# Optimization experiments

Measured on AMD Instinct MI355X. Metric: run time of the kernel, lower is better.

## Reference

```python
import jax, jax.numpy as jnp
import numpy as np
from functools import partial

GRID = 5  # 224/32 - 2
N_ANCHORS = 3
N_BOX = GRID * GRID * N_ANCHORS  # 75


def _make_anchors():
    # faithful replication of _create_anchors (grid-index cx,cy with pixel-scale w,h)
    scales = [56, 112, 224]
    a = np.zeros((GRID, GRID, N_ANCHORS, 8), np.float32)
    for x in range(GRID):
        for y in range(GRID):
            for k in range(N_ANCHORS):
                w = h = scales[k]
                a[x, y, k] = [x - w // 2, y - h // 2, x + w // 2, y + h // 2, x, y, w, h]
    return jnp.asarray(a)

ANCHORS = _make_anchors()  # [5,5,3,8]: x0,y0,x1,y1,cx,cy,w,h


def conv2d(x, w, b, pad):
    y = jax.lax.conv_general_dilated(x, w, (1, 1), [(pad, pad), (pad, pad)],
                                     dimension_numbers=('NCHW', 'OIHW', 'NCHW'))
    return y + b[None, :, None, None]


def maxpool2(x):
    return jax.lax.reduce_window(x, -jnp.inf, jax.lax.max,
                                 (1, 1, 2, 2), (1, 1, 2, 2), 'VALID')


def deparam_bboxes(rp_reg):
    # rp_reg: [B,5,5,3,4]; anchors broadcast over batch
    aw = ANCHORS[..., 6]; ah = ANCHORS[..., 7]
    ax = ANCHORS[..., 4]; ay = ANCHORS[..., 5]
    cx = rp_reg[..., 0] * aw + ax
    cy = rp_reg[..., 1] * ah + ay
    w = jnp.exp(rp_reg[..., 2]) * aw
    h = jnp.exp(rp_reg[..., 3]) * ah
    return jnp.stack([cx - w / 2, cy - h / 2, cx + w / 2, cy + h / 2], axis=-1)


def _iou_as_written(bi, bj):
    # replicates bb_intersection_over_union EXACTLY, including the missing
    # parentheses bug: inter/areaA + areaB - inter
    xA = jnp.maximum(bi[0], bj[..., 0]); yA = jnp.maximum(bi[1], bj[..., 1])
    xB = jnp.minimum(bi[2], bj[..., 2]); yB = jnp.minimum(bi[3], bj[..., 3])
    inter = jnp.maximum(0.0, xB - xA + 1) * jnp.maximum(0.0, yB - yA + 1)
    areaA = (bi[2] - bi[0] + 1) * (bi[3] - bi[1] + 1)
    areaB = (bj[..., 2] - bj[..., 0] + 1) * (bj[..., 3] - bj[..., 1] + 1)
    return inter / areaA + areaB - inter


def nms_single(boxes, scores, thresh=0.7):
    # boxes [75,4], scores [75]; greedy suppression in score order (vectorized
    # replacement of the O(n^2) Python-loop NMS in _compute_bboxes)
    order = jnp.argsort(-scores)
    b = boxes[order]
    idx = jnp.arange(N_BOX)

    def body(i, keep):
        iou = _iou_as_written(b[i], b)          # [75]
        sup = (idx > i) & (iou > thresh) & keep[i]
        return keep & ~sup

    keep_sorted = jax.lax.fori_loop(0, N_BOX, body, jnp.ones(N_BOX, bool))
    return jnp.zeros(N_BOX, bool).at[order].set(keep_sorted)


def setup_inputs() -> dict:
    key = jax.random.key(0)
    ks = jax.random.split(key, 16)
    B = 32
    inp = {"x": jax.random.normal(ks[0], (B, 3, 224, 224), jnp.float32)}
    chans = [3, 64, 128, 256, 512, 512]
    for i in range(5):
        cin, cout = chans[i], chans[i + 1]
        std = float(np.sqrt(2.0 / (cout * 9)))  # kaiming fan_out, relu
        inp[f"fw{i}"] = jax.random.normal(ks[1 + i], (cout, cin, 3, 3), jnp.float32) * std
        inp[f"fb{i}"] = jnp.zeros((cout,), jnp.float32)
    # RPN heads: normal(0, 0.01), zero bias (per _initialize_rp_weights)
    inp["rpw_w"] = jax.random.normal(ks[6], (512, 512, 3, 3), jnp.float32) * 0.01
    inp["rpw_b"] = jnp.zeros((512,), jnp.float32)
    inp["cls_w"] = jax.random.normal(ks[7], (N_ANCHORS, 512, 1, 1), jnp.float32) * 0.01
    inp["cls_b"] = jnp.zeros((N_ANCHORS,), jnp.float32)
    inp["reg_w"] = jax.random.normal(ks[8], (4 * N_ANCHORS, 512, 1, 1), jnp.float32) * 0.01
    inp["reg_b"] = jnp.zeros((4 * N_ANCHORS,), jnp.float32)
    # classifier2: Linear(512*7*7, 20), normal(0, 0.01)
    inp["fc_w"] = jax.random.normal(ks[9], (20, 512 * 7 * 7), jnp.float32) * 0.01
    inp["fc_b"] = jnp.zeros((20,), jnp.float32)
    return inp


def reference(x, fw0, fb0, fw1, fb1, fw2, fb2, fw3, fb3, fw4, fb4,
              rpw_w, rpw_b, cls_w, cls_b, reg_w, reg_b, fc_w, fc_b):
    B = x.shape[0]
    feat = x
    for w, b in ((fw0, fb0), (fw1, fb1), (fw2, fb2), (fw3, fb3), (fw4, fb4)):
        feat = maxpool2(jax.nn.relu(conv2d(feat, w, b, pad=1)))
    # feat: [B,512,7,7]
    rp512 = jax.nn.relu(conv2d(feat, rpw_w, rpw_b, pad=0))          # [B,512,5,5]
    rp_cls = jax.nn.sigmoid(conv2d(rp512, cls_w, cls_b, pad=0))     # [B,3,5,5]
    rp_reg = conv2d(rp512, reg_w, reg_b, pad=0)                     # [B,12,5,5]
    # faithful to torch .view (row-major reshape, NOT permute)
    rp_cls = rp_cls.reshape(B, GRID, GRID, N_ANCHORS)
    rp_reg = rp_reg.reshape(B, GRID, GRID, N_ANCHORS, 4)
    bboxes = deparam_bboxes(rp_reg)                                 # [B,5,5,3,4]
    keep = jax.vmap(nms_single)(bboxes.reshape(B, N_BOX, 4),
                                rp_cls.reshape(B, N_BOX))           # [B,75] bool
    logits = feat.reshape(B, -1) @ fc_w.T + fc_b                    # [B,20]
    return logits, rp_cls, rp_reg, bboxes, keep
```

## Files before the change

### kernel.cpp

```cpp
#include <hip/hip_runtime.h>
#include <math.h>


#define OFF_LOGITS 0
#define OFF_CLS    640
#define OFF_REG    3040
#define OFF_BOXES  12640
#define OFF_KEEP   22240

constexpr int BATCH = 32;

typedef _Float16 h8 __attribute__((ext_vector_type(8)));
typedef _Float16 h4 __attribute__((ext_vector_type(4)));
typedef float    f4 __attribute__((ext_vector_type(4)));

#define MFMA16(a, b, c) __builtin_amdgcn_mfma_f32_16x16x32_f16(a, b, c, 0, 0, 0)

#if defined(__has_builtin)
#  if __has_builtin(__builtin_amdgcn_global_load_lds)
#    define HAS_GLL 1
#  endif
#endif

__device__ __forceinline__ void stage16(const _Float16* g, _Float16* lbase, int lane) {
#ifdef HAS_GLL
  __builtin_amdgcn_global_load_lds((const __attribute__((address_space(1))) void*)g,
                                   (__attribute__((address_space(3))) void*)lbase,
                                   16, 0, 0);
#else
  *reinterpret_cast<h8*>(lbase + lane * 8) = *reinterpret_cast<const h8*>(g);
#endif
}

constexpr size_t A_OFF = 0;
constexpr size_t B_OFF = 106463232;
constexpr size_t W_OFF = 161579008;
constexpr size_t P_OFF = A_OFF + 8388608;

constexpr int I0_E = 26615808;
constexpr int I1_E = 13778944;
constexpr int I2_E = 7372800;
constexpr int I3_E = 4194304;
constexpr int I4_E = 802816;

__global__ __launch_bounds__(256)
void wcvt(const float* __restrict__ src, _Float16* __restrict__ dHi,
          _Float16* __restrict__ dLo, int COUT, int CIN) {
  const int total = COUT * CIN * 9;
  for (int idx = blockIdx.x * 256 + threadIdx.x; idx < total; idx += gridDim.x * 256) {
    const int co = idx / (CIN * 9);
    const int r = idx % (CIN * 9);
    const int ci = r / 9, tap = r % 9;
    const float v = src[idx];
    const _Float16 h = (_Float16)v;
    const int o = ((tap * (CIN >> 5) + (ci >> 5)) * COUT + co) * 32 + (ci & 31);
    dHi[o] = h;
    dLo[o] = (_Float16)(v - (float)h);
  }
}

__global__ __launch_bounds__(256)
void zero_ring(_Float16* __restrict__ hi, _Float16* __restrict__ lo, int P, int C) {
  const int c8n = C / 8, cells = 4 * P - 4;
  const int tot = 32 * cells * c8n;
  for (int idx = blockIdx.x * 256 + threadIdx.x; idx < tot; idx += gridDim.x * 256) {
    const int c8 = idx % c8n;
    const int cell = (idx / c8n) % cells;
    const int n = idx / (c8n * cells);
    int y, xx;
    if (cell < 2 * P) { y = (cell < P) ? 0 : (P - 1); xx = cell % P; }
    else { const int q = cell - 2 * P; y = 1 + (q >> 1); xx = (q & 1) ? (P - 1) : 0; }
    const long o = ((long)(n * P + y) * P + xx) * C + c8 * 8;
    h8 z = {};
    *reinterpret_cast<h8*>(hi + o) = z;
    *reinterpret_cast<h8*>(lo + o) = z;
  }
}

__global__ __launch_bounds__(256)
void conv_l0(const float* __restrict__ x, const float* __restrict__ w0,
             const float* __restrict__ b0, _Float16* __restrict__ outHi,
             _Float16* __restrict__ outLo) {
  const int bid = blockIdx.x;
  const int tx0 = (bid % 7) * 16, ty0 = ((bid / 7) % 7) * 16, n = bid / 49;
  __shared__ float sIn[3 * 34 * 34];
  __shared__ float sW[1728];
  __shared__ float sB[64];
  const int tid = threadIdx.x;
  for (int idx = tid; idx < 3 * 34 * 34; idx += 256) {
    const int ci = idx / 1156, rem = idx % 1156, r = rem / 34, cc = rem % 34;
    const int y = 2 * ty0 - 1 + r, xx = 2 * tx0 - 1 + cc;
    float v = 0.f;
    if ((unsigned)y < 224u && (unsigned)xx < 224u)
      v = x[((n * 3 + ci) * 224 + y) * 224 + xx];
    sIn[idx] = v;
  }
  for (int idx = tid; idx < 1728; idx += 256) sW[idx] = w0[idx];
  if (tid < 64) sB[tid] = b0[tid];
  __syncthreads();

  const int tpy = tid / 16, tpx = tid % 16;
  float win[3][4][4];
  #pragma unroll
  for (int ci = 0; ci < 3; ++ci)
    #pragma unroll
    for (int dr = 0; dr < 4; ++dr)
      #pragma unroll
      for (int dc = 0; dc < 4; ++dc)
        win[ci][dr][dc] = sIn[ci * 1156 + (2 * tpy + dr) * 34 + (2 * tpx + dc)];

  const long ob = ((long)(n * 114 + ty0 + tpy + 1) * 114 + tx0 + tpx + 1) * 64;
  for (int co4 = 0; co4 < 16; ++co4) {
    h4 hh, ll;
    #pragma unroll
    for (int j = 0; j < 4; ++j) {
      const int co = co4 * 4 + j;
      float a00 = 0.f, a01 = 0.f, a10 = 0.f, a11 = 0.f;
      #pragma unroll
      for (int ci = 0; ci < 3; ++ci)
        #pragma unroll
        for (int ky = 0; ky < 3; ++ky)
          #pragma unroll
          for (int kx = 0; kx < 3; ++kx) {
            const float wv = sW[co * 27 + ci * 9 + ky * 3 + kx];
            a00 = fmaf(win[ci][ky][kx], wv, a00);
            a01 = fmaf(win[ci][ky][kx + 1], wv, a01);
            a10 = fmaf(win[ci][ky + 1][kx], wv, a10);
            a11 = fmaf(win[ci][ky + 1][kx + 1], wv, a11);
          }
      const float p = fmaxf(fmaxf(fmaxf(a00, a01), fmaxf(a10, a11)) + sB[co], 0.f);
      const _Float16 h = (_Float16)p;
      hh[j] = h;
      ll[j] = (_Float16)(p - (float)h);
    }
    *reinterpret_cast<h4*>(outHi + ob + co4 * 4) = hh;
    *reinterpret_cast<h4*>(outLo + ob + co4 * 4) = ll;
  }
}

template<int CIN, int COUT, int H, int BCO, int BSP, int TG, int KPH, int MODE>
__global__ __launch_bounds__(256, 2)
void convpool(const _Float16* __restrict__ inHi, const _Float16* __restrict__ inLo,
              const _Float16* __restrict__ wHi, const _Float16* __restrict__ wLo,
              const float* __restrict__ bias, _Float16* __restrict__ outHi,
              _Float16* __restrict__ outLo, float* __restrict__ outF) {
  constexpr int W = H, Hp = H / 2, Wp = W / 2, PW = W + 2, POW = Wp + 2;
  constexpr int NCOW = BCO / 64, NSPW = BSP / 64;
  static_assert(NCOW * NSPW == 4, "4 waves");
  constexpr int KCH = CIN / 32;
  constexpr int NCH = TG * KCH;
  constexpr int NPH = NCH / KPH;
  static_assert(NCH % KPH == 0, "even phases");
  constexpr int NISS = BSP / 64;
  constexpr int SPTOT = 32 * H * W;
  constexpr int TSZ = BSP * 32;
  __align__(16) __shared__ _Float16 sB[2 * 2 * KPH * TSZ];
  #define TIDX(buf, hl, j) ((((buf) * 2 + (hl)) * KPH + (j)) * TSZ)

  const int tid = threadIdx.x;
  const int lane = tid & 63, wv = tid >> 6;
  const int c = lane & 15, kq = lane >> 4;
  const int cow = blockIdx.y * BCO + (wv % NCOW) * 64;
  const int spl = (wv / NCOW) * 64;
  const int sblk = blockIdx.x * BSP;
  const int tap0 = (TG == 9) ? 0 : blockIdx.z * TG;

  int gstage[NISS];
  #pragma unroll
  for (int i = 0; i < NISS; ++i) {
    const int sl = i * 64 + tid / 4;
    const int sg = sblk + sl;
    const int ry = sg & 1, tt = sg >> 1;
    const int x = tt % W, u = tt / W;
    const int py = u % Hp, n = u / Hp;
    gstage[i] = ((n * (H + 2) + 2 * py + ry) * PW + x) * CIN +
                (((tid & 3) ^ ((sl >> 1) & 3)) * 8);
  }
  int dsoff[4];
  #pragma unroll
  for (int nt = 0; nt < 4; ++nt) {
    const int row = spl + nt * 16 + c;
    dsoff[nt] = row * 32 + ((kq ^ ((row >> 1) & 3)) * 8);
  }

  #pragma unroll
  for (int j = 0; j < KPH; ++j) {
    const int tap = tap0 + j / KCH, kc = j % KCH;
    const int tb = ((tap / 3) * PW + (tap % 3)) * CIN + kc * 32;
    #pragma unroll
    for (int i = 0; i < NISS; ++i) {
      stage16(inHi + gstage[i] + tb, &sB[TIDX(0, 0, j) + i * 2048 + wv * 512], lane);
      stage16(inLo + gstage[i] + tb, &sB[TIDX(0, 1, j) + i * 2048 + wv * 512], lane);
    }
  }
  __syncthreads();

  f4 acc[4][4] = {};
  int cur = 0;
  for (int ph = 0; ph < NPH; ++ph) {
    h8 aH[KPH][4], aL[KPH][4];
    #pragma unroll
    for (int j = 0; j < KPH; ++j) {
      const int ch = ph * KPH + j;
      const int tap = tap0 + ch / KCH;
      const int kc = ch % KCH;
      const long abase = ((long)(tap * KCH + kc) * COUT + cow) * 32;
      #pragma unroll
      for (int mt = 0; mt < 4; ++mt) {
        const long ao = abase + (mt * 16 + c) * 32 + kq * 8;
        aH[j][mt] = *reinterpret_cast<const h8*>(wHi + ao);
        aL[j][mt] = *reinterpret_cast<const h8*>(wLo + ao);
      }
    }
    if (ph + 1 < NPH) {
      #pragma unroll
      for (int j2 = 0; j2 < KPH; ++j2) {
        const int ch2 = (ph + 1) * KPH + j2;
        const int tap2 = tap0 + ch2 / KCH;
        const int tb2 = ((tap2 / 3) * PW + (tap2 % 3)) * CIN + (ch2 % KCH) * 32;
        #pragma unroll
        for (int i = 0; i < NISS; ++i) {
          stage16(inHi + gstage[i] + tb2,
                  &sB[TIDX(cur ^ 1, 0, j2) + i * 2048 + wv * 512], lane);
          stage16(inLo + gstage[i] + tb2,
                  &sB[TIDX(cur ^ 1, 1, j2) + i * 2048 + wv * 512], lane);
        }
      }
    }
    #pragma unroll
    for (int j = 0; j < KPH; ++j) {
      h8 bH[4], bL[4];
      #pragma unroll
      for (int nt = 0; nt < 4; ++nt) {
        bH[nt] = *reinterpret_cast<const h8*>(&sB[TIDX(cur, 0, j) + dsoff[nt]]);
        bL[nt] = *reinterpret_cast<const h8*>(&sB[TIDX(cur, 1, j) + dsoff[nt]]);
      }
      __builtin_amdgcn_s_setprio(1);
      #pragma unroll
      for (int mt = 0; mt < 4; ++mt)
        #pragma unroll
        for (int nt = 0; nt < 4; ++nt)
          acc[mt][nt] = MFMA16(aH[j][mt], bH[nt], acc[mt][nt]);
      #pragma unroll
      for (int mt = 0; mt < 4; ++mt)
        #pragma unroll
        for (int nt = 0; nt < 4; ++nt)
          acc[mt][nt] = MFMA16(aH[j][mt], bL[nt], acc[mt][nt]);
      #pragma unroll
      for (int mt = 0; mt < 4; ++mt)
        #pragma unroll
        for (int nt = 0; nt < 4; ++nt)
          acc[mt][nt] = MFMA16(aL[j][mt], bH[nt], acc[mt][nt]);
      __builtin_amdgcn_s_setprio(0);
    }
    __syncthreads();
    cur ^= 1;
  }
  #undef TIDX

  const int r4 = lane >> 4;
  if (MODE == 1) {
    #pragma unroll
    for (int mt = 0; mt < 4; ++mt) {
      const int co0 = cow + mt * 16 + r4 * 4;
      #pragma unroll
      for (int nt = 0; nt < 4; ++nt) {
        const int s = sblk + spl + nt * 16 + c;
        *reinterpret_cast<f4*>(outF + ((long)blockIdx.z * SPTOT + s) * COUT + co0) =
            acc[mt][nt];
      }
    }
  } else {
    #pragma unroll
    for (int mt = 0; mt < 4; ++mt) {
      const int co0 = cow + mt * 16 + r4 * 4;
      const f4 bi = *reinterpret_cast<const f4*>(bias + co0);
      #pragma unroll
      for (int nt = 0; nt < 4; ++nt) {
        f4 v = acc[mt][nt];
        #pragma unroll
        for (int r = 0; r < 4; ++r) {
          const float m1 = fmaxf(v[r], __shfl_xor(v[r], 1, 64));
          v[r] = fmaxf(m1, __shfl_xor(m1, 2, 64));
        }
        if ((lane & 3) == 0) {
          const int s = sblk + spl + nt * 16 + c;
          const int ps = s >> 2;
          const int n = ps / (Hp * Wp), rem = ps % (Hp * Wp);
          const int py = rem / Wp, px = rem % Wp;
          h4 hh, ll;
          #pragma unroll
          for (int r = 0; r < 4; ++r) {
            const float p = fmaxf(v[r] + bi[r], 0.f);
            const _Float16 h = (_Float16)p;
            hh[r] = h;
            ll[r] = (_Float16)(p - (float)h);
          }
          const long oa = ((long)((n * (Hp + 2) + py + 1) * POW + px + 1)) * COUT + co0;
          *reinterpret_cast<h4*>(outHi + oa) = hh;
          *reinterpret_cast<h4*>(outLo + oa) = ll;
        }
      }
    }
  }
}

__global__ __launch_bounds__(256)
void l4_finish(const float* __restrict__ part, const float* __restrict__ bias,
               _Float16* __restrict__ I4h, _Float16* __restrict__ I4l,
               float* __restrict__ feat) {
  const int t = blockIdx.x * 256 + threadIdx.x;
  if (t >= 1568 * 128) return;
  const int co0 = (t % 128) * 4, p = t / 128;
  f4 m;
  #pragma unroll
  for (int q = 0; q < 4; ++q) {
    const long s = 4L * p + q;
    f4 v = *reinterpret_cast<const f4*>(part + s * 512 + co0);
    v += *reinterpret_cast<const f4*>(part + (6272 + s) * 512 + co0);
    v += *reinterpret_cast<const f4*>(part + (12544 + s) * 512 + co0);
    if (q == 0) m = v;
    else {
      #pragma unroll
      for (int r = 0; r < 4; ++r) m[r] = fmaxf(m[r], v[r]);
    }
  }
  const f4 bi = *reinterpret_cast<const f4*>(bias + co0);
  h4 hh, ll;
  const int n = p / 49, pix = p % 49;
  #pragma unroll
  for (int r = 0; r < 4; ++r) {
    const float pv = fmaxf(m[r] + bi[r], 0.f);
    const _Float16 h = (_Float16)pv;
    hh[r] = h;
    ll[r] = (_Float16)(pv - (float)h);
    feat[((long)(n * 512 + co0 + r)) * 49 + pix] = pv;
  }
  *reinterpret_cast<h4*>(I4h + (long)p * 512 + co0) = hh;
  *reinterpret_cast<h4*>(I4l + (long)p * 512 + co0) = ll;
}

__global__ __launch_bounds__(256)
void rpn_partial(const _Float16* __restrict__ inHi, const _Float16* __restrict__ inLo,
                 const _Float16* __restrict__ wHi, const _Float16* __restrict__ wLo,
                 float* __restrict__ part) {
  const int lane = threadIdx.x & 63, wv = threadIdx.x >> 6;
  const int cow = blockIdx.y * 128 + wv * 32;
  const int sblk = blockIdx.x * 64;
  const int tap = blockIdx.z, ky = tap / 3, kx = tap % 3;
  const int c = lane & 15, kq = lane >> 4;

  int baseB[4];
  #pragma unroll
  for (int nt = 0; nt < 4; ++nt) {
    int s = sblk + nt * 16 + c;
    if (s > 799) s = 799;
    const int n = s / 25, pix = s % 25, py = pix / 5, px = pix % 5;
    baseB[nt] = ((n * 7 + py + ky) * 7 + px + kx) * 512;
  }

  f4 acc[2][4] = {};
  for (int kch = 0; kch < 16; ++kch) {
    h8 aH[2], aL[2], bH[4], bL[4];
    const long abase = ((long)(tap * 16 + kch) * 512 + cow) * 32;
    #pragma unroll
    for (int mt = 0; mt < 2; ++mt) {
      const long ao = abase + (mt * 16 + c) * 32 + kq * 8;
      aH[mt] = *reinterpret_cast<const h8*>(wHi + ao);
      aL[mt] = *reinterpret_cast<const h8*>(wLo + ao);
    }
    #pragma unroll
    for (int nt = 0; nt < 4; ++nt) {
      const int bo = baseB[nt] + kch * 32 + kq * 8;
      bH[nt] = *reinterpret_cast<const h8*>(inHi + bo);
      bL[nt] = *reinterpret_cast<const h8*>(inLo + bo);
    }
    #pragma unroll
    for (int mt = 0; mt < 2; ++mt)
      #pragma unroll
      for (int nt = 0; nt < 4; ++nt)
        acc[mt][nt] = MFMA16(aH[mt], bH[nt], acc[mt][nt]);
    #pragma unroll
    for (int mt = 0; mt < 2; ++mt)
      #pragma unroll
      for (int nt = 0; nt < 4; ++nt)
        acc[mt][nt] = MFMA16(aH[mt], bL[nt], acc[mt][nt]);
    #pragma unroll
    for (int mt = 0; mt < 2; ++mt)
      #pragma unroll
      for (int nt = 0; nt < 4; ++nt)
        acc[mt][nt] = MFMA16(aL[mt], bH[nt], acc[mt][nt]);
  }

  const int r4 = lane >> 4;
  #pragma unroll
  for (int mt = 0; mt < 2; ++mt) {
    const int co0 = cow + mt * 16 + r4 * 4;
    #pragma unroll
    for (int nt = 0; nt < 4; ++nt) {
      const int s = sblk + nt * 16 + c;
      if (s < 800)
        *reinterpret_cast<f4*>(part + ((long)tap * 800 + s) * 512 + co0) = acc[mt][nt];
    }
  }
}

__global__ __launch_bounds__(256)
void rpn_finish(const float* __restrict__ part, const float* __restrict__ bias,
                float* __restrict__ rp512) {
  const int t = blockIdx.x * 256 + threadIdx.x;
  if (t >= 800 * 128) return;
  const int co0 = (t % 128) * 4, s = t / 128;
  f4 acc = *reinterpret_cast<const f4*>(bias + co0);
  #pragma unroll
  for (int g = 0; g < 9; ++g)
    acc += *reinterpret_cast<const f4*>(part + ((long)g * 800 + s) * 512 + co0);
  f4 o;
  #pragma unroll
  for (int r = 0; r < 4; ++r) o[r] = fmaxf(acc[r], 0.f);
  *reinterpret_cast<f4*>(rp512 + (long)s * 512 + co0) = o;
}

__global__ __launch_bounds__(256)
void heads_kernel(const float* __restrict__ rp512,
                  const float* __restrict__ cls_w, const float* __restrict__ cls_b,
                  const float* __restrict__ reg_w, const float* __restrict__ reg_b,
                  float* __restrict__ out) {
  const int idx = blockIdx.x * 256 + threadIdx.x;
  if (idx >= 32 * 25 * 15) return;
  const int o = idx % 15, pix = (idx / 15) % 25, n = idx / 375;
  const float* __restrict__ ip = rp512 + ((long)(n * 25 + pix)) * 512;
  const float* __restrict__ wvp = (o < 3) ? (cls_w + o * 512) : (reg_w + (o - 3) * 512);
  float acc = 0.f;
  for (int k = 0; k < 512; k += 4) {
    const f4 a = *reinterpret_cast<const f4*>(ip + k);
    const f4 b = *reinterpret_cast<const f4*>(wvp + k);
    acc = fmaf(a[0], b[0], acc); acc = fmaf(a[1], b[1], acc);
    acc = fmaf(a[2], b[2], acc); acc = fmaf(a[3], b[3], acc);
  }
  if (o < 3) {
    acc += cls_b[o];
    out[OFF_CLS + n * 75 + o * 25 + pix] = 1.f / (1.f + expf(-acc));
  } else {
    acc += reg_b[o - 3];
    out[OFF_REG + n * 300 + (o - 3) * 25 + pix] = acc;
  }
}

__global__ __launch_bounds__(256)
void fc_kernel(const float* __restrict__ feat, const float* __restrict__ fw,
               const float* __restrict__ fb, float* __restrict__ out) {
  const int n = blockIdx.x, j = blockIdx.y;
  const float* __restrict__ ip = feat + (long)n * 25088;
  const float* __restrict__ wj = fw + (long)j * 25088;
  float acc = 0.f;
  for (int k = threadIdx.x * 4; k < 25088; k += 1024) {
    const f4 a = *reinterpret_cast<const f4*>(ip + k);
    const f4 b = *reinterpret_cast<const f4*>(wj + k);
    acc = fmaf(a[0], b[0], acc); acc = fmaf(a[1], b[1], acc);
    acc = fmaf(a[2], b[2], acc); acc = fmaf(a[3], b[3], acc);
  }
  #pragma unroll
  for (int m = 32; m >= 1; m >>= 1) acc += __shfl_xor(acc, m, 64);
  __shared__ float red[4];
  const int wv = threadIdx.x >> 6;
  if ((threadIdx.x & 63) == 0) red[wv] = acc;
  __syncthreads();
  if (threadIdx.x == 0)
    out[OFF_LOGITS + n * 20 + j] = red[0] + red[1] + red[2] + red[3] + fb[j];
}

__global__ __launch_bounds__(128)
void bbox_nms_kernel(float* __restrict__ out) {
  const int n = blockIdx.x;
  const int t = threadIdx.x;
  __shared__ float bx0[75], by0[75], bx1[75], by1[75], area[75], sc[75];
  __shared__ int rank_s[75], order_s[75], keep_s[75];

  if (t < 75) {
    const int g1 = t / 15, g2 = (t / 3) % 5, a = t % 3;
    const float aw = (a == 0) ? 56.f : (a == 1 ? 112.f : 224.f);
    const float r0 = out[OFF_REG + n * 300 + 4 * t + 0];
    const float r1 = out[OFF_REG + n * 300 + 4 * t + 1];
    const float r2 = out[OFF_REG + n * 300 + 4 * t + 2];
    const float r3 = out[OFF_REG + n * 300 + 4 * t + 3];
    const float cx = r0 * aw + (float)g1;
    const float cy = r1 * aw + (float)g2;
    const float w_ = expf(r2) * aw;
    const float h_ = expf(r3) * aw;
    const float x0 = cx - 0.5f * w_, y0 = cy - 0.5f * h_;
    const float x1 = cx + 0.5f * w_, y1 = cy + 0.5f * h_;
    bx0[t] = x0; by0[t] = y0; bx1[t] = x1; by1[t] = y1;
    area[t] = (x1 - x0 + 1.f) * (y1 - y0 + 1.f);
    out[OFF_BOXES + n * 300 + 4 * t + 0] = x0;
    out[OFF_BOXES + n * 300 + 4 * t + 1] = y0;
    out[OFF_BOXES + n * 300 + 4 * t + 2] = x1;
    out[OFF_BOXES + n * 300 + 4 * t + 3] = y1;
    sc[t] = out[OFF_CLS + n * 75 + t];
    keep_s[t] = 1;
  }
  __syncthreads();
  if (t < 75) {
    const float si = sc[t];
    int rk = 0;
    for (int j = 0; j < 75; ++j) {
      const float sj = sc[j];
      rk += (sj > si) || (sj == si && j < t);
    }
    rank_s[t] = rk;
    order_s[rk] = t;
  }
  __syncthreads();
  for (int i = 0; i < 74; ++i) {
    if (keep_s[i]) {
      const int bi = order_s[i];
      if (t > i && t < 75) {
        const int bj = order_s[t];
        const float xA = fmaxf(bx0[bi], bx0[bj]);
        const float yA = fmaxf(by0[bi], by0[bj]);
        const float xB = fminf(bx1[bi], bx1[bj]);
        const float yB = fminf(by1[bi], by1[bj]);
        const float inter = fmaxf(0.f, xB - xA + 1.f) * fmaxf(0.f, yB - yA + 1.f);
        const float iou = inter / area[bi] + area[bj] - inter;
        if (iou > 0.7f) keep_s[t] = 0;
      }
    }
    __syncthreads();
  }
  if (t < 75) out[OFF_KEEP + n * 75 + t] = keep_s[rank_s[t]] ? 1.f : 0.f;
}

extern "C" void kernel_launch(void* const* d_in, const int* in_sizes, int n_in,
                              void* d_out, int out_size, void* d_ws, size_t ws_size,
                              hipStream_t stream) {
  (void)in_sizes; (void)n_in; (void)out_size; (void)ws_size;
  const float* x     = (const float*)d_in[0];
  const float* fw0   = (const float*)d_in[1];
  const float* fb0   = (const float*)d_in[2];
  const float* fw1   = (const float*)d_in[3];
  const float* fb1   = (const float*)d_in[4];
  const float* fw2   = (const float*)d_in[5];
  const float* fb2   = (const float*)d_in[6];
  const float* fw3   = (const float*)d_in[7];
  const float* fb3   = (const float*)d_in[8];
  const float* fw4   = (const float*)d_in[9];
  const float* fb4   = (const float*)d_in[10];
  const float* rpw_w = (const float*)d_in[11];
  const float* rpw_b = (const float*)d_in[12];
  const float* cls_w = (const float*)d_in[13];
  const float* cls_b = (const float*)d_in[14];
  const float* reg_w = (const float*)d_in[15];
  const float* reg_b = (const float*)d_in[16];
  const float* fc_w  = (const float*)d_in[17];
  const float* fc_b  = (const float*)d_in[18];
  float* out = (float*)d_out;
  char* ws = (char*)d_ws;

  _Float16* I0h = (_Float16*)(ws + A_OFF);
  _Float16* I0l = I0h + I0_E;
  _Float16* I1h = (_Float16*)(ws + B_OFF);
  _Float16* I1l = I1h + I1_E;
  _Float16* I2h = (_Float16*)(ws + A_OFF);
  _Float16* I2l = I2h + I2_E;
  _Float16* I3h = (_Float16*)(ws + B_OFF);
  _Float16* I3l = I3h + I3_E;
  _Float16* I4h = (_Float16*)(ws + A_OFF);
  _Float16* I4l = I4h + I4_E;
  float* feat  = (float*)(ws + A_OFF + (size_t)I4_E * 4);
  float* rp512 = (float*)(ws + A_OFF + (size_t)I4_E * 4 + 3211264);
  float* part  = (float*)(ws + P_OFF);

  _Float16* w1h = (_Float16*)(ws + W_OFF);                _Float16* w1l = w1h + 73728;
  _Float16* w2h = (_Float16*)(ws + W_OFF + 294912);       _Float16* w2l = w2h + 294912;
  _Float16* w3h = (_Float16*)(ws + W_OFF + 1474560);      _Float16* w3l = w3h + 1179648;
  _Float16* w4h = (_Float16*)(ws + W_OFF + 6193152);      _Float16* w4l = w4h + 2359296;
  _Float16* wrh = (_Float16*)(ws + W_OFF + 15630336);     _Float16* wrl = wrh + 2359296;

  wcvt<<<(73728 + 255) / 256, 256, 0, stream>>>(fw1, w1h, w1l, 128, 64);
  wcvt<<<(294912 + 255) / 256, 256, 0, stream>>>(fw2, w2h, w2l, 256, 128);
  wcvt<<<(1179648 + 255) / 256, 256, 0, stream>>>(fw3, w3h, w3l, 512, 256);
  wcvt<<<(2359296 + 255) / 256, 256, 0, stream>>>(fw4, w4h, w4l, 512, 512);
  wcvt<<<(2359296 + 255) / 256, 256, 0, stream>>>(rpw_w, wrh, wrl, 512, 512);

  zero_ring<<<512, 256, 0, stream>>>(I0h, I0l, 114, 64);
  zero_ring<<<512, 256, 0, stream>>>(I1h, I1l, 58, 128);

  conv_l0<<<32 * 49, 256, 0, stream>>>(x, fw0, fb0, I0h, I0l);

  convpool<64, 128, 112, 128, 128, 9, 1, 0><<<dim3(3136, 1, 1), 256, 0, stream>>>(
      I0h, I0l, w1h, w1l, fb1, I1h, I1l, nullptr);
  zero_ring<<<512, 256, 0, stream>>>(I2h, I2l, 30, 256);
  convpool<128, 256, 56, 256, 64, 9, 2, 0><<<dim3(1568, 1, 1), 256, 0, stream>>>(
      I1h, I1l, w2h, w2l, fb2, I2h, I2l, nullptr);
  zero_ring<<<512, 256, 0, stream>>>(I3h, I3l, 16, 512);
  convpool<256, 512, 28, 256, 64, 9, 2, 0><<<dim3(392, 2, 1), 256, 0, stream>>>(
      I2h, I2l, w3h, w3l, fb3, I3h, I3l, nullptr);
  convpool<512, 512, 14, 256, 64, 3, 2, 1><<<dim3(98, 2, 3), 256, 0, stream>>>(
      I3h, I3l, w4h, w4l, nullptr, nullptr, nullptr, part);
  l4_finish<<<(1568 * 128 + 255) / 256, 256, 0, stream>>>(part, fb4, I4h, I4l, feat);

  rpn_partial<<<dim3(13, 4, 9), 256, 0, stream>>>(I4h, I4l, wrh, wrl, part);
  rpn_finish<<<(800 * 128 + 255) / 256, 256, 0, stream>>>(part, rpw_b, rp512);

  heads_kernel<<<(12000 + 255) / 256, 256, 0, stream>>>(rp512, cls_w, cls_b, reg_w, reg_b, out);
  fc_kernel<<<dim3(32, 20), 256, 0, stream>>>(feat, fc_w, fc_b, out);
  bbox_nms_kernel<<<BATCH, 128, 0, stream>>>(out);
}
```

Before: 1.002 ms.

## Add row-tiled convrow kernel reusing staged input across kx taps for layers 1-3

Adds a convrow kernel in which each block handles one output row pair (two input rows by the padded width) and stages one ky row of input per phase. All three kx taps are then read from that shared tile through shifted LDS offsets, so input staging traffic drops roughly threefold compared with staging each of the nine taps separately. The 2x2 max-pool is done inside registers with lane shuffles before bias, ReLU and the split-fp16 store. Layers 1-3 switch to this kernel, and sched_barrier fences are also added around the staging code in the existing convpool. The cost is edge padding waste in the spatial tile, clamped indices, and a different grid shape that may change occupancy and the balance between weight loads and input reuse.

New measurement: 1.023 ms. 2.1% more time.

```diff
diff --git a/kernel.cpp b/kernel.cpp
--- a/kernel.cpp
+++ b/kernel.cpp
@@ -135,6 +135,145 @@
     }
     *reinterpret_cast<h4*>(outHi + ob + co4 * 4) = hh;
     *reinterpret_cast<h4*>(outLo + ob + co4 * 4) = ll;
+  }
+}
+
+template<int CIN, int COUT, int H, int XPAD>
+__global__ __launch_bounds__(256, 2)
+void convrow(const _Float16* __restrict__ inHi, const _Float16* __restrict__ inLo,
+             const _Float16* __restrict__ wHi, const _Float16* __restrict__ wLo,
+             const float* __restrict__ bias, _Float16* __restrict__ outHi,
+             _Float16* __restrict__ outLo) {
+  constexpr int W = H, Hp = H / 2, Wp = W / 2, PW = W + 2, POW = Wp + 2;
+  constexpr int BSP = XPAD * 2;
+  constexpr int NSPW = BSP / 64;
+  constexpr int NCOW = 4 / NSPW;
+  constexpr int BCO = NCOW * 64;
+  constexpr int KCH = CIN / 32;
+  constexpr int NPH = 3 * KCH;
+  constexpr int NISS = BSP / 64;
+  __align__(16) __shared__ _Float16 sB[2][2][BSP * 32];
+
+  const int tid = threadIdx.x;
+  const int lane = tid & 63, wv = tid >> 6;
+  const int c = lane & 15, kq = lane >> 4;
+  const int cow = blockIdx.y * BCO + (wv % NCOW) * 64;
+  const int spl = (wv / NCOW) * 64;
+  const int py = blockIdx.x % Hp, n = blockIdx.x / Hp;
+
+  int gstage[NISS];
+  #pragma unroll
+  for (int i = 0; i < NISS; ++i) {
+    const int sl = i * 64 + tid / 4;
+    const int ry = sl & 1;
+    int xx = sl >> 1;
+    if (xx > PW - 1) xx = PW - 1;
+    gstage[i] = ((n * (H + 2) + 2 * py + ry) * PW + xx) * CIN +
+                (((tid & 3) ^ ((sl >> 1) & 3)) * 8);
+  }
+  int dsoff[3][4];
+  #pragma unroll
+  for (int kx = 0; kx < 3; ++kx)
+    #pragma unroll
+    for (int nt = 0; nt < 4; ++nt) {
+      int r = spl + nt * 16 + c + 2 * kx;
+      if (r > BSP - 1) r = BSP - 1;
+      dsoff[kx][nt] = r * 32 + ((kq ^ ((r >> 1) & 3)) * 8);
+    }
+
+  #pragma unroll
+  for (int i = 0; i < NISS; ++i) {
+    stage16(inHi + gstage[i], &sB[0][0][i * 2048 + wv * 512], lane);
+    stage16(inLo + gstage[i], &sB[0][1][i * 2048 + wv * 512], lane);
+  }
+  __syncthreads();
+
+  f4 acc[4][4] = {};
+  int cur = 0;
+  for (int ph = 0; ph < NPH; ++ph) {
+    const int ky = ph / KCH, kc = ph % KCH;
+    h8 aH[3][4], aL[3][4];
+    #pragma unroll
+    for (int kx = 0; kx < 3; ++kx) {
+      const long abase = ((long)((ky * 3 + kx) * KCH + kc) * COUT + cow) * 32;
+      #pragma unroll
+      for (int mt = 0; mt < 4; ++mt) {
+        const long ao = abase + (mt * 16 + c) * 32 + kq * 8;
+        aH[kx][mt] = *reinterpret_cast<const h8*>(wHi + ao);
+        aL[kx][mt] = *reinterpret_cast<const h8*>(wLo + ao);
+      }
+    }
+    __builtin_amdgcn_sched_barrier(0);
+    if (ph + 1 < NPH) {
+      const int tb2 = ((ph + 1) / KCH) * PW * CIN + ((ph + 1) % KCH) * 32;
+      #pragma unroll
+      for (int i = 0; i < NISS; ++i) {
+        stage16(inHi + gstage[i] + tb2, &sB[cur ^ 1][0][i * 2048 + wv * 512], lane);
+        stage16(inLo + gstage[i] + tb2, &sB[cur ^ 1][1][i * 2048 + wv * 512], lane);
+      }
+    }
+    __builtin_amdgcn_sched_barrier(0);
+    #pragma unroll
+    for (int kx = 0; kx < 3; ++kx) {
+      h8 bH[4], bL[4];
+      #pragma unroll
+      for (int nt = 0; nt < 4; ++nt) {
+        bH[nt] = *reinterpret_cast<const h8*>(&sB[cur][0][dsoff[kx][nt]]);
+        bL[nt] = *reinterpret_cast<const h8*>(&sB[cur][1][dsoff[kx][nt]]);
+      }
+      __builtin_amdgcn_s_setprio(1);
+      #pragma unroll
+      for (int mt = 0; mt < 4; ++mt)
+        #pragma unroll
+        for (int nt = 0; nt < 4; ++nt)
+          acc[mt][nt] = MFMA16(aH[kx][mt], bH[nt], acc[mt][nt]);
+      #pragma unroll
+      for (int mt = 0; mt < 4; ++mt)
+        #pragma unroll
+        for (int nt = 0; nt < 4; ++nt)
+          acc[mt][nt] = MFMA16(aH[kx][mt], bL[nt], acc[mt][nt]);
+      #pragma unroll
+      for (int mt = 0; mt < 4; ++mt)
+        #pragma unroll
+        for (int nt = 0; nt < 4; ++nt)
+          acc[mt][nt] = MFMA16(aL[kx][mt], bH[nt], acc[mt][nt]);
+      __builtin_amdgcn_s_setprio(0);
+    }
+    __syncthreads();
+    cur ^= 1;
+  }
+
+  const int r4 = lane >> 4;
+  #pragma unroll
+  for (int mt = 0; mt < 4; ++mt) {
+    const int co0 = cow + mt * 16 + r4 * 4;
+    const f4 bi = *reinterpret_cast<const f4*>(bias + co0);
+    #pragma unroll
+    for (int nt = 0; nt < 4; ++nt) {
+      f4 v = acc[mt][nt];
+      #pragma unroll
+      for (int r = 0; r < 4; ++r) {
+        const float m1 = fmaxf(v[r], __shfl_xor(v[r], 1, 64));
+        v[r] = fmaxf(m1, __shfl_xor(m1, 2, 64));
+      }
+      if ((lane & 3) == 0) {
+        const int rr = spl + nt * 16 + c;
+        const int px = rr >> 2;
+        if (px < Wp) {
+          h4 hh, ll;
+          #pragma unroll
+          for (int r = 0; r < 4; ++r) {
+            const float p = fmaxf(v[r] + bi[r], 0.f);
+            const _Float16 h = (_Float16)p;
+            hh[r] = h;
+            ll[r] = (_Float16)(p - (float)h);
+          }
+          const long oa = ((long)((n * (Hp + 2) + py + 1) * POW + px + 1)) * COUT + co0;
+          *reinterpret_cast<h4*>(outHi + oa) = hh;
+          *reinterpret_cast<h4*>(outLo + oa) = ll;
+        }
+      }
+    }
   }
 }
 
@@ -212,6 +351,7 @@
         aL[j][mt] = *reinterpret_cast<const h8*>(wLo + ao);
       }
     }
+    __builtin_amdgcn_sched_barrier(0);
     if (ph + 1 < NPH) {
       #pragma unroll
       for (int j2 = 0; j2 < KPH; ++j2) {
@@ -227,6 +367,7 @@
         }
       }
     }
+    __builtin_amdgcn_sched_barrier(0);
     #pragma unroll
     for (int j = 0; j < KPH; ++j) {
       h8 bH[4], bL[4];
@@ -587,14 +728,14 @@
 
   conv_l0<<<32 * 49, 256, 0, stream>>>(x, fw0, fb0, I0h, I0l);
 
-  convpool<64, 128, 112, 128, 128, 9, 1, 0><<<dim3(3136, 1, 1), 256, 0, stream>>>(
-      I0h, I0l, w1h, w1l, fb1, I1h, I1l, nullptr);
+  convrow<64, 128, 112, 128><<<dim3(32 * 56, 2), 256, 0, stream>>>(
+      I0h, I0l, w1h, w1l, fb1, I1h, I1l);
   zero_ring<<<512, 256, 0, stream>>>(I2h, I2l, 30, 256);
-  convpool<128, 256, 56, 256, 64, 9, 2, 0><<<dim3(1568, 1, 1), 256, 0, stream>>>(
-      I1h, I1l, w2h, w2l, fb2, I2h, I2l, nullptr);
+  convrow<128, 256, 56, 64><<<dim3(32 * 28, 2), 256, 0, stream>>>(
+      I1h, I1l, w2h, w2l, fb2, I2h, I2l);
   zero_ring<<<512, 256, 0, stream>>>(I3h, I3l, 16, 512);
-  convpool<256, 512, 28, 256, 64, 9, 2, 0><<<dim3(392, 2, 1), 256, 0, stream>>>(
-      I2h, I2l, w3h, w3l, fb3, I3h, I3l, nullptr);
+  convrow<256, 512, 28, 32><<<dim3(32 * 14, 2), 256, 0, stream>>>(
+      I2h, I2l, w3h, w3l, fb3, I3h, I3l);
   convpool<512, 512, 14, 256, 64, 3, 2, 1><<<dim3(98, 2, 3), 256, 0, stream>>>(
       I3h, I3l, w4h, w4l, nullptr, nullptr, nullptr, part);
   l4_finish<<<(1568 * 128 + 255) / 256, 256, 0, stream>>>(part, fb4, I4h, I4l, feat);
```

## Triple-buffer conv input staging with two-phase-ahead prefetch and explicit vmcnt waits

Applied to the files above, without the earlier changes.

Moves the convpool kernel's LDS input staging from double to triple buffering, so global-to-LDS copies run two phases ahead of the MFMA consumer instead of one. The prologue stages two phases, then waits with a hand-written vmcnt and an s_barrier rather than a full __syncthreads. Scheduling barriers pin the order of weight loads, staging and compute. The goal is to hide more global load latency behind the MFMA work. The cost is 1.5x LDS per block, which may reduce occupancy. The synchronisation also relies on the in-order vmcnt counter and a hardcoded wait literal, which is fragile.

After: 1.008 ms. About the same (+0.6%).

```diff
diff --git a/kernel.cpp b/kernel.cpp
--- a/kernel.cpp
+++ b/kernel.cpp
@@ -151,10 +151,11 @@
   constexpr int NCH = TG * KCH;
   constexpr int NPH = NCH / KPH;
   static_assert(NCH % KPH == 0, "even phases");
+  static_assert(KPH * 2 * (BSP / 64) == 4, "prologue vmcnt literal = 4");
   constexpr int NISS = BSP / 64;
   constexpr int SPTOT = 32 * H * W;
   constexpr int TSZ = BSP * 32;
-  __align__(16) __shared__ _Float16 sB[2 * 2 * KPH * TSZ];
+  __align__(16) __shared__ _Float16 sB[3 * 2 * KPH * TSZ];
   #define TIDX(buf, hl, j) ((((buf) * 2 + (hl)) * KPH + (j)) * TSZ)
 
   const int tid = threadIdx.x;
@@ -184,20 +185,28 @@
   }
 
   #pragma unroll
-  for (int j = 0; j < KPH; ++j) {
-    const int tap = tap0 + j / KCH, kc = j % KCH;
-    const int tb = ((tap / 3) * PW + (tap % 3)) * CIN + kc * 32;
-    #pragma unroll
-    for (int i = 0; i < NISS; ++i) {
-      stage16(inHi + gstage[i] + tb, &sB[TIDX(0, 0, j) + i * 2048 + wv * 512], lane);
-      stage16(inLo + gstage[i] + tb, &sB[TIDX(0, 1, j) + i * 2048 + wv * 512], lane);
-    }
-  }
-  __syncthreads();
+  for (int pp = 0; pp < 2; ++pp) {
+    #pragma unroll
+    for (int j = 0; j < KPH; ++j) {
+      const int ch = pp * KPH + j;
+      const int tap = tap0 + ch / KCH, kc = ch % KCH;
+      const int tb = ((tap / 3) * PW + (tap % 3)) * CIN + kc * 32;
+      #pragma unroll
+      for (int i = 0; i < NISS; ++i) {
+        stage16(inHi + gstage[i] + tb, &sB[TIDX(pp, 0, j) + i * 2048 + wv * 512], lane);
+        stage16(inLo + gstage[i] + tb, &sB[TIDX(pp, 1, j) + i * 2048 + wv * 512], lane);
+      }
+    }
+  }
+  __builtin_amdgcn_sched_barrier(0);
+  asm volatile("s_waitcnt vmcnt(4)" ::: "memory");
+  __builtin_amdgcn_sched_barrier(0);
+  __builtin_amdgcn_s_barrier();
+  __builtin_amdgcn_sched_barrier(0);
 
   f4 acc[4][4] = {};
-  int cur = 0;
   for (int ph = 0; ph < NPH; ++ph) {
+    const int bp = ph % 3;
     h8 aH[KPH][4], aL[KPH][4];
     #pragma unroll
     for (int j = 0; j < KPH; ++j) {
@@ -212,28 +221,31 @@
         aL[j][mt] = *reinterpret_cast<const h8*>(wLo + ao);
       }
     }
-    if (ph + 1 < NPH) {
+    __builtin_amdgcn_sched_barrier(0);
+    if (ph + 2 < NPH) {
+      const int bs = (ph + 2) % 3;
       #pragma unroll
       for (int j2 = 0; j2 < KPH; ++j2) {
-        const int ch2 = (ph + 1) * KPH + j2;
+        const int ch2 = (ph + 2) * KPH + j2;
         const int tap2 = tap0 + ch2 / KCH;
         const int tb2 = ((tap2 / 3) * PW + (tap2 % 3)) * CIN + (ch2 % KCH) * 32;
         #pragma unroll
         for (int i = 0; i < NISS; ++i) {
           stage16(inHi + gstage[i] + tb2,
-                  &sB[TIDX(cur ^ 1, 0, j2) + i * 2048 + wv * 512], lane);
+                  &sB[TIDX(bs, 0, j2) + i * 2048 + wv * 512], lane);
           stage16(inLo + gstage[i] + tb2,
-                  &sB[TIDX(cur ^ 1, 1, j2) + i * 2048 + wv * 512], lane);
+                  &sB[TIDX(bs, 1, j2) + i * 2048 + wv * 512], lane);
         }
       }
     }
+    __builtin_amdgcn_sched_barrier(0);
     #pragma unroll
     for (int j = 0; j < KPH; ++j) {
       h8 bH[4], bL[4];
       #pragma unroll
       for (int nt = 0; nt < 4; ++nt) {
-        bH[nt] = *reinterpret_cast<const h8*>(&sB[TIDX(cur, 0, j) + dsoff[nt]]);
-        bL[nt] = *reinterpret_cast<const h8*>(&sB[TIDX(cur, 1, j) + dsoff[nt]]);
+        bH[nt] = *reinterpret_cast<const h8*>(&sB[TIDX(bp, 0, j) + dsoff[nt]]);
+        bL[nt] = *reinterpret_cast<const h8*>(&sB[TIDX(bp, 1, j) + dsoff[nt]]);
       }
       __builtin_amdgcn_s_setprio(1);
       #pragma unroll
@@ -253,8 +265,9 @@
           acc[mt][nt] = MFMA16(aL[j][mt], bH[nt], acc[mt][nt]);
       __builtin_amdgcn_s_setprio(0);
     }
-    __syncthreads();
-    cur ^= 1;
+    __builtin_amdgcn_sched_barrier(0);
+    __builtin_amdgcn_s_barrier();
+    __builtin_amdgcn_sched_barrier(0);
   }
   #undef TIDX
 
```
